# Kernel optimization log

Hardware: AMD Instinct MI355X
Metric: run time of the kernel (lower is better)

The kernel has to match this reference:

```python
import jax, jax.numpy as jnp
import numpy as np

B, C, T, S = 128, 64, 8192, 16

def setup_inputs() -> dict:
    key = jax.random.key(0)
    k1, k2, k3, k4 = jax.random.split(key, 4)
    x = jax.random.normal(k1, (B, C, T), dtype=jnp.float32)
    subj_idx = jax.random.randint(k2, (B,), 0, S)
    # per-subject 1x1 conv == per-subject [C, C] matrix + bias.
    # (original identity-inits; we use identity + small noise so the op is non-trivial)
    W = jnp.eye(C, dtype=jnp.float32)[None] + 0.02 * jax.random.normal(k3, (S, C, C), dtype=jnp.float32)
    b = 0.02 * jax.random.normal(k4, (S, C), dtype=jnp.float32)
    return {"x": x, "subj_idx": subj_idx, "W": W, "b": b}

def reference(x, subj_idx, W, b):
    # Hard routing: gather each sample's subject weight, then batched 1x1 conv.
    Wb = W[subj_idx]            # [B, C_out, C_in]
    bb = b[subj_idx]            # [B, C_out]
    # out[b, o, t] = sum_c Wb[b, o, c] * x[b, c, t] + bb[b, o]
    return jnp.einsum('boc,bct->bot', Wb, x) + bb[:, :, None]
```

## Files before the change

### kernel.cpp

```cpp
#include <hip/hip_runtime.h>
#include <hip/hip_bf16.h>


typedef __attribute__((ext_vector_type(8))) short  bf16x8;
typedef __attribute__((ext_vector_type(16))) float f32x16;

namespace {
constexpr int Cdim  = 64;
constexpr int Tdim  = 8192;
constexpr int TT    = 256;
constexpr int BLOCK = 256;
}

static __device__ __forceinline__ unsigned short f2bfu(float f) {
    return __builtin_bit_cast(unsigned short, __float2bfloat16(f));
}
static __device__ __forceinline__ float bf2f(unsigned short u) {
    const unsigned int v = ((unsigned int)u) << 16;
    return __builtin_bit_cast(float, v);
}

__global__ __launch_bounds__(BLOCK, 4)
void subject_layers_r9(const float* __restrict__ x,
                       const int*   __restrict__ subj,
                       const float* __restrict__ W,
                       const float* __restrict__ bias,
                       float*       __restrict__ out) {
    __shared__ unsigned short tile[Cdim * TT];

    const int b    = blockIdx.y;
    const int tb   = blockIdx.x;
    const int tid  = threadIdx.x;
    const int wave = tid >> 6;
    const int lane = tid & 63;
    const int hi   = lane >> 5;
    const int ln   = lane & 31;
    const int s    = subj[b];

    const size_t xbase = (size_t)b * Cdim * Tdim + (size_t)tb * TT;

    {
        float4 v[4];
        #pragma unroll
        for (int gg = 0; gg < 4; ++gg) {
            #pragma unroll
            for (int g = 0; g < 4; ++g) {
                const int row = (gg * 4 + g) * 4 + wave;
                v[g] = *reinterpret_cast<const float4*>(
                    x + xbase + (size_t)row * Tdim + lane * 4);
            }
            #pragma unroll
            for (int g = 0; g < 4; ++g) {
                const int row = (gg * 4 + g) * 4 + wave;
                ushort4 u;
                u.x = f2bfu(v[g].x); u.y = f2bfu(v[g].y);
                u.z = f2bfu(v[g].z); u.w = f2bfu(v[g].w);
                *reinterpret_cast<ushort4*>(&tile[row * TT + lane * 4]) = u;
            }
        }
    }

    bf16x8 afrag[2][4];
    const float* Wb = W + (size_t)s * Cdim * Cdim;
    #pragma unroll
    for (int ot = 0; ot < 2; ++ot) {
        #pragma unroll
        for (int kb = 0; kb < 4; ++kb) {
            const float* ap = Wb + (size_t)(ot * 32 + ln) * Cdim + kb * 16 + hi * 8;
            const float4 a0 = *reinterpret_cast<const float4*>(ap);
            const float4 a1 = *reinterpret_cast<const float4*>(ap + 4);
            bf16x8 f;
            f[0] = (short)f2bfu(a0.x); f[1] = (short)f2bfu(a0.y);
            f[2] = (short)f2bfu(a0.z); f[3] = (short)f2bfu(a0.w);
            f[4] = (short)f2bfu(a1.x); f[5] = (short)f2bfu(a1.y);
            f[6] = (short)f2bfu(a1.z); f[7] = (short)f2bfu(a1.w);
            afrag[ot][kb] = f;
        }
    }

    f32x16 bini[2];
    const float* bb = bias + (size_t)s * Cdim;
    #pragma unroll
    for (int ot = 0; ot < 2; ++ot)
        #pragma unroll
        for (int r = 0; r < 16; ++r)
            bini[ot][r] = bb[ot * 32 + (r & 3) + 8 * (r >> 2) + 4 * hi];

    __syncthreads();

    #pragma unroll
    for (int st = 0; st < 2; ++st) {
        const int col = wave * 64 + st * 32 + ln;

        bf16x8 bfrag[4];
        #pragma unroll
        for (int kb = 0; kb < 4; ++kb) {
            bf16x8 f;
            #pragma unroll
            for (int j = 0; j < 8; ++j)
                f[j] = (short)tile[(kb * 16 + hi * 8 + j) * TT + col];
            bfrag[kb] = f;
        }

        #pragma unroll
        for (int ot = 0; ot < 2; ++ot) {
            f32x16 acc = bini[ot];
            #pragma unroll
            for (int kb = 0; kb < 4; ++kb)
                acc = __builtin_amdgcn_mfma_f32_32x32x16_bf16(
                    afrag[ot][kb], bfrag[kb], acc, 0, 0, 0);
            #pragma unroll
            for (int r = 0; r < 16; ++r)
                tile[(ot * 32 + (r & 3) + 8 * (r >> 2) + 4 * hi) * TT + col] =
                    f2bfu(acc[r]);
        }
    }

    __syncthreads();

    #pragma unroll
    for (int g = 0; g < 16; ++g) {
        const int row = g * 4 + wave;
        const ushort4 u = *reinterpret_cast<const ushort4*>(&tile[row * TT + lane * 4]);
        float4 o4;
        o4.x = bf2f(u.x); o4.y = bf2f(u.y); o4.z = bf2f(u.z); o4.w = bf2f(u.w);
        *reinterpret_cast<float4*>(out + xbase + (size_t)row * Tdim + lane * 4) = o4;
    }
}

extern "C" void kernel_launch(void* const* d_in, const int* in_sizes, int n_in,
                              void* d_out, int out_size, void* d_ws, size_t ws_size,
                              hipStream_t stream) {
    const float* x    = (const float*)d_in[0];
    const int*   subj = (const int*)  d_in[1];
    const float* W    = (const float*)d_in[2];
    const float* bias = (const float*)d_in[3];
    float*       out  = (float*)d_out;

    const int B = in_sizes[1];
    dim3 grid(Tdim / TT, B);
    dim3 block(BLOCK);
    hipLaunchKernelGGL(subject_layers_r9, grid, block, 0, stream,
                       x, subj, W, bias, out);
}
```

Measured before the change: 104.9 us.

## Double time tile and store MFMA results directly to global memory

Doubles the time tile per block from 256 to 512 columns, lowering launch bounds to 2 blocks per SM because LDS use doubles. Drops the shared-memory staging and bf16 round-trip of the output: each lane writes fp32 accumulators straight to global, 32 consecutive columns per row per half-wave. This removes a sync, an LDS pass and a bf16 rounding of the output. The direct stores are only 128-byte coalesced segments spread over many rows, and the larger tile lowers occupancy.

```diff
diff --git a/kernel.cpp b/kernel.cpp
--- a/kernel.cpp
+++ b/kernel.cpp
@@ -8,24 +8,20 @@
 namespace {
 constexpr int Cdim  = 64;
 constexpr int Tdim  = 8192;
-constexpr int TT    = 256;
+constexpr int TT    = 512;
 constexpr int BLOCK = 256;
 }
 
 static __device__ __forceinline__ unsigned short f2bfu(float f) {
     return __builtin_bit_cast(unsigned short, __float2bfloat16(f));
 }
-static __device__ __forceinline__ float bf2f(unsigned short u) {
-    const unsigned int v = ((unsigned int)u) << 16;
-    return __builtin_bit_cast(float, v);
-}
 
-__global__ __launch_bounds__(BLOCK, 4)
-void subject_layers_r9(const float* __restrict__ x,
-                       const int*   __restrict__ subj,
-                       const float* __restrict__ W,
-                       const float* __restrict__ bias,
-                       float*       __restrict__ out) {
+__global__ __launch_bounds__(BLOCK, 2)
+void subject_layers_r11(const float* __restrict__ x,
+                        const int*   __restrict__ subj,
+                        const float* __restrict__ W,
+                        const float* __restrict__ bias,
+                        float*       __restrict__ out) {
     __shared__ unsigned short tile[Cdim * TT];
 
     const int b    = blockIdx.y;
@@ -40,22 +36,26 @@
     const size_t xbase = (size_t)b * Cdim * Tdim + (size_t)tb * TT;
 
     {
-        float4 v[4];
+        float4 v0[4], v1[4];
         #pragma unroll
         for (int gg = 0; gg < 4; ++gg) {
             #pragma unroll
             for (int g = 0; g < 4; ++g) {
                 const int row = (gg * 4 + g) * 4 + wave;
-                v[g] = *reinterpret_cast<const float4*>(
-                    x + xbase + (size_t)row * Tdim + lane * 4);
+                const float* rp = x + xbase + (size_t)row * Tdim;
+                v0[g] = *reinterpret_cast<const float4*>(rp + lane * 4);
+                v1[g] = *reinterpret_cast<const float4*>(rp + 256 + lane * 4);
             }
             #pragma unroll
             for (int g = 0; g < 4; ++g) {
                 const int row = (gg * 4 + g) * 4 + wave;
-                ushort4 u;
-                u.x = f2bfu(v[g].x); u.y = f2bfu(v[g].y);
-                u.z = f2bfu(v[g].z); u.w = f2bfu(v[g].w);
-                *reinterpret_cast<ushort4*>(&tile[row * TT + lane * 4]) = u;
+                ushort4 u0, u1;
+                u0.x = f2bfu(v0[g].x); u0.y = f2bfu(v0[g].y);
+                u0.z = f2bfu(v0[g].z); u0.w = f2bfu(v0[g].w);
+                u1.x = f2bfu(v1[g].x); u1.y = f2bfu(v1[g].y);
+                u1.z = f2bfu(v1[g].z); u1.w = f2bfu(v1[g].w);
+                *reinterpret_cast<ushort4*>(&tile[row * TT + lane * 4]) = u0;
+                *reinterpret_cast<ushort4*>(&tile[row * TT + 256 + lane * 4]) = u1;
             }
         }
     }
@@ -88,9 +88,10 @@
 
     __syncthreads();
 
+    float* ob = out + xbase;
     #pragma unroll
-    for (int st = 0; st < 2; ++st) {
-        const int col = wave * 64 + st * 32 + ln;
+    for (int st = 0; st < 4; ++st) {
+        const int col = wave * 128 + st * 32 + ln;
 
         bf16x8 bfrag[4];
         #pragma unroll
@@ -111,20 +112,9 @@
                     afrag[ot][kb], bfrag[kb], acc, 0, 0, 0);
             #pragma unroll
             for (int r = 0; r < 16; ++r)
-                tile[(ot * 32 + (r & 3) + 8 * (r >> 2) + 4 * hi) * TT + col] =
-                    f2bfu(acc[r]);
+                ob[(size_t)(ot * 32 + (r & 3) + 8 * (r >> 2) + 4 * hi) * Tdim + col]
+                    = acc[r];
         }
-    }
-
-    __syncthreads();
-
-    #pragma unroll
-    for (int g = 0; g < 16; ++g) {
-        const int row = g * 4 + wave;
-        const ushort4 u = *reinterpret_cast<const ushort4*>(&tile[row * TT + lane * 4]);
-        float4 o4;
-        o4.x = bf2f(u.x); o4.y = bf2f(u.y); o4.z = bf2f(u.z); o4.w = bf2f(u.w);
-        *reinterpret_cast<float4*>(out + xbase + (size_t)row * Tdim + lane * 4) = o4;
     }
 }
 
@@ -140,6 +130,6 @@
     const int B = in_sizes[1];
     dim3 grid(Tdim / TT, B);
     dim3 block(BLOCK);
-    hipLaunchKernelGGL(subject_layers_r9, grid, block, 0, stream,
+    hipLaunchKernelGGL(subject_layers_r11, grid, block, 0, stream,
                        x, subj, W, bias, out);
 }
```

New measurement: 116.1 us. 10.7% more time.

## Pipeline x loads over K-chunks with MFMA and store fp32 accumulators directly

Applied to the files above, without the earlier changes.

Splits the input channel dimension into four 16-row chunks and overlaps the global load of the next chunk with MFMA work on the current one, keeping accumulators for both column subtiles live across chunks. Output is written directly from the fp32 accumulators to global memory instead of round-tripping through bf16 shared memory. This removes the bf16 rounding of the output and the second LDS pass, but the direct stores have a strided per-lane pattern (32 columns contiguous per row) and more registers are needed, so launch bounds are lowered to 2 blocks per SIMD hint.

```diff
diff --git a/kernel.cpp b/kernel.cpp
--- a/kernel.cpp
+++ b/kernel.cpp
@@ -15,17 +15,13 @@
 static __device__ __forceinline__ unsigned short f2bfu(float f) {
     return __builtin_bit_cast(unsigned short, __float2bfloat16(f));
 }
-static __device__ __forceinline__ float bf2f(unsigned short u) {
-    const unsigned int v = ((unsigned int)u) << 16;
-    return __builtin_bit_cast(float, v);
-}
 
-__global__ __launch_bounds__(BLOCK, 4)
-void subject_layers_r9(const float* __restrict__ x,
-                       const int*   __restrict__ subj,
-                       const float* __restrict__ W,
-                       const float* __restrict__ bias,
-                       float*       __restrict__ out) {
+__global__ __launch_bounds__(BLOCK, 2)
+void subject_layers_r13(const float* __restrict__ x,
+                        const int*   __restrict__ subj,
+                        const float* __restrict__ W,
+                        const float* __restrict__ bias,
+                        float*       __restrict__ out) {
     __shared__ unsigned short tile[Cdim * TT];
 
     const int b    = blockIdx.y;
@@ -39,25 +35,12 @@
 
     const size_t xbase = (size_t)b * Cdim * Tdim + (size_t)tb * TT;
 
-    {
-        float4 v[4];
-        #pragma unroll
-        for (int gg = 0; gg < 4; ++gg) {
-            #pragma unroll
-            for (int g = 0; g < 4; ++g) {
-                const int row = (gg * 4 + g) * 4 + wave;
-                v[g] = *reinterpret_cast<const float4*>(
-                    x + xbase + (size_t)row * Tdim + lane * 4);
-            }
-            #pragma unroll
-            for (int g = 0; g < 4; ++g) {
-                const int row = (gg * 4 + g) * 4 + wave;
-                ushort4 u;
-                u.x = f2bfu(v[g].x); u.y = f2bfu(v[g].y);
-                u.z = f2bfu(v[g].z); u.w = f2bfu(v[g].w);
-                *reinterpret_cast<ushort4*>(&tile[row * TT + lane * 4]) = u;
-            }
-        }
+    float4 v[4];
+
+    #pragma unroll
+    for (int g = 0; g < 4; ++g) {
+        const int row = 0 * 16 + g * 4 + wave;
+        v[g] = *reinterpret_cast<const float4*>(x + xbase + (size_t)row * Tdim + lane * 4);
     }
 
     bf16x8 afrag[2][4];
@@ -78,53 +61,79 @@
         }
     }
 
-    f32x16 bini[2];
-    const float* bb = bias + (size_t)s * Cdim;
+    f32x16 acc[2][2];
+    {
+        const float* bb = bias + (size_t)s * Cdim;
+        #pragma unroll
+        for (int ot = 0; ot < 2; ++ot) {
+            f32x16 bi;
+            #pragma unroll
+            for (int r = 0; r < 16; ++r)
+                bi[r] = bb[ot * 32 + (r & 3) + 8 * (r >> 2) + 4 * hi];
+            acc[0][ot] = bi;
+            acc[1][ot] = bi;
+        }
+    }
+
     #pragma unroll
-    for (int ot = 0; ot < 2; ++ot)
-        #pragma unroll
-        for (int r = 0; r < 16; ++r)
-            bini[ot][r] = bb[ot * 32 + (r & 3) + 8 * (r >> 2) + 4 * hi];
-
+    for (int g = 0; g < 4; ++g) {
+        const int row = 0 * 16 + g * 4 + wave;
+        ushort4 u;
+        u.x = f2bfu(v[g].x); u.y = f2bfu(v[g].y);
+        u.z = f2bfu(v[g].z); u.w = f2bfu(v[g].w);
+        *reinterpret_cast<ushort4*>(&tile[row * TT + lane * 4]) = u;
+    }
     __syncthreads();
 
     #pragma unroll
-    for (int st = 0; st < 2; ++st) {
-        const int col = wave * 64 + st * 32 + ln;
+    for (int q = 1; q < 4; ++q) {
+        #pragma unroll
+        for (int g = 0; g < 4; ++g) {
+            const int row = q * 16 + g * 4 + wave;
+            v[g] = *reinterpret_cast<const float4*>(x + xbase + (size_t)row * Tdim + lane * 4);
+        }
 
-        bf16x8 bfrag[4];
         #pragma unroll
-        for (int kb = 0; kb < 4; ++kb) {
+        for (int st = 0; st < 2; ++st) {
+            const int col = wave * 64 + st * 32 + ln;
             bf16x8 f;
             #pragma unroll
             for (int j = 0; j < 8; ++j)
-                f[j] = (short)tile[(kb * 16 + hi * 8 + j) * TT + col];
-            bfrag[kb] = f;
+                f[j] = (short)tile[((q - 1) * 16 + hi * 8 + j) * TT + col];
+            #pragma unroll
+            for (int ot = 0; ot < 2; ++ot)
+                acc[st][ot] = __builtin_amdgcn_mfma_f32_32x32x16_bf16(
+                    afrag[ot][q - 1], f, acc[st][ot], 0, 0, 0);
         }
 
         #pragma unroll
+        for (int g = 0; g < 4; ++g) {
+            const int row = q * 16 + g * 4 + wave;
+            ushort4 u;
+            u.x = f2bfu(v[g].x); u.y = f2bfu(v[g].y);
+            u.z = f2bfu(v[g].z); u.w = f2bfu(v[g].w);
+            *reinterpret_cast<ushort4*>(&tile[row * TT + lane * 4]) = u;
+        }
+        __syncthreads();
+    }
+
+    float* ob = out + xbase;
+    #pragma unroll
+    for (int st = 0; st < 2; ++st) {
+        const int col = wave * 64 + st * 32 + ln;
+        bf16x8 f;
+        #pragma unroll
+        for (int j = 0; j < 8; ++j)
+            f[j] = (short)tile[(3 * 16 + hi * 8 + j) * TT + col];
+        #pragma unroll
         for (int ot = 0; ot < 2; ++ot) {
-            f32x16 acc = bini[ot];
-            #pragma unroll
-            for (int kb = 0; kb < 4; ++kb)
-                acc = __builtin_amdgcn_mfma_f32_32x32x16_bf16(
-                    afrag[ot][kb], bfrag[kb], acc, 0, 0, 0);
+            acc[st][ot] = __builtin_amdgcn_mfma_f32_32x32x16_bf16(
+                afrag[ot][3], f, acc[st][ot], 0, 0, 0);
             #pragma unroll
             for (int r = 0; r < 16; ++r)
-                tile[(ot * 32 + (r & 3) + 8 * (r >> 2) + 4 * hi) * TT + col] =
-                    f2bfu(acc[r]);
+                ob[(size_t)(ot * 32 + (r & 3) + 8 * (r >> 2) + 4 * hi) * Tdim + col]
+                    = acc[st][ot][r];
         }
-    }
-
-    __syncthreads();
-
-    #pragma unroll
-    for (int g = 0; g < 16; ++g) {
-        const int row = g * 4 + wave;
-        const ushort4 u = *reinterpret_cast<const ushort4*>(&tile[row * TT + lane * 4]);
-        float4 o4;
-        o4.x = bf2f(u.x); o4.y = bf2f(u.y); o4.z = bf2f(u.z); o4.w = bf2f(u.w);
-        *reinterpret_cast<float4*>(out + xbase + (size_t)row * Tdim + lane * 4) = o4;
     }
 }
 
@@ -140,6 +149,6 @@
     const int B = in_sizes[1];
     dim3 grid(Tdim / TT, B);
     dim3 block(BLOCK);
-    hipLaunchKernelGGL(subject_layers_r9, grid, block, 0, stream,
+    hipLaunchKernelGGL(subject_layers_r13, grid, block, 0, stream,
                        x, subj, W, bias, out);
 }
```

After: 105.8 us. No clear change (+0.9%).
